# Kernel tuning notes

Hardware: AMD Instinct MI355X
Metric: run time of the kernel (lower is better)

## Reference

```python
import jax, jax.numpy as jnp
import numpy as np

B, T, D, O, E = 4, 4096, 256, 256, 16


def setup_inputs() -> dict:
    key = jax.random.key(0)
    ks = jax.random.split(key, 5)
    s_in = 1.0 / np.sqrt(D)
    x = jax.random.normal(ks[0], (B, T, D), dtype=jnp.float32)
    We = jax.random.uniform(ks[1], (E, D, O), minval=-s_in, maxval=s_in, dtype=jnp.float32)
    be = jax.random.uniform(ks[2], (E, O), minval=-s_in, maxval=s_in, dtype=jnp.float32)
    Wg = jax.random.uniform(ks[3], (D, E), minval=-s_in, maxval=s_in, dtype=jnp.float32)
    bg = jax.random.uniform(ks[4], (E,), minval=-s_in, maxval=s_in, dtype=jnp.float32)
    return {"x": x, "We": We, "be": be, "Wg": Wg, "bg": bg}


def reference(x, We, be, Wg, bg):
    # gate: softmax over experts  [B,T,E]
    gate = jax.nn.softmax(jnp.einsum("btd,de->bte", x, Wg) + bg, axis=-1)
    # all experts: batched GEMM  [B,T,E,O]
    h = jax.nn.gelu(jnp.einsum("btd,edo->bteo", x, We) + be, approximate=False)
    # softmax-weighted sum over experts  [B,T,O]
    return jnp.einsum("bteo,bte->bto", h, gate)
```

## Files before the change

### kernel.cpp

```cpp
#include <hip/hip_runtime.h>
#include <stdint.h>

#define KD 256
#define NO 256
#define NE 16
#define BM 64
#define BN 128
#define XROW 264
#define NFRAG 128

typedef short bf16x8 __attribute__((ext_vector_type(8)));
typedef float f32x4 __attribute__((ext_vector_type(4)));

__device__ __forceinline__ unsigned short f2bf(float f) {
  uint32_t u = __float_as_uint(f);
  u += 0x7fffu + ((u >> 16) & 1u);
  return (unsigned short)(u >> 16);
}
__device__ __forceinline__ float bf2f(unsigned short h) {
  return __uint_as_float(((uint32_t)h) << 16);
}
__device__ __forceinline__ float gelu_f(float h) {
  float z = h * fmaf(0.07135481627f, h * h, 1.5957691216f);
  return h * __builtin_amdgcn_rcpf(1.0f + __expf(-z));
}

__global__ void moe_prep(const float* __restrict__ We, unsigned short* __restrict__ Wf,
                         const float* __restrict__ Wg, unsigned short* __restrict__ Wgt)
{
  __shared__ float ts[256 * 17];
  const int tid = threadIdx.x;
  const int bid = blockIdx.x;
  if (bid < 256) {
    const int e = bid >> 4, ob = bid & 15;
    const float* src = We + (size_t)e * KD * NO + ob * 16;
    const int o = tid & 15, dg = tid >> 4;
#pragma unroll
    for (int p = 0; p < 16; ++p) {
      int d = p * 16 + dg;
      ts[d * 17 + o] = src[(size_t)d * NO + o];
    }
    __syncthreads();
    const int w = tid >> 6, l = tid & 63;
    const int q = l >> 4, ln = l & 15;
#pragma unroll
    for (int kk = 0; kk < 2; ++kk) {
      int kc = w + kk * 4;
      unsigned int pk[4];
#pragma unroll
      for (int h = 0; h < 4; ++h) {
        unsigned short lo = f2bf(ts[(kc * 32 + q * 8 + h * 2 + 0) * 17 + ln]);
        unsigned short hi = f2bf(ts[(kc * 32 + q * 8 + h * 2 + 1) * 17 + ln]);
        pk[h] = (unsigned int)lo | ((unsigned int)hi << 16);
      }
      uint4* dst = (uint4*)(Wf + ((((size_t)(e * 8 + kc) * 16 + ob) * 64) + l) * 8);
      *dst = make_uint4(pk[0], pk[1], pk[2], pk[3]);
    }
  } else {
    int d = tid;
    const float* wr = Wg + (size_t)d * NE;
#pragma unroll
    for (int e = 0; e < NE; ++e)
      Wgt[e * KD + d] = f2bf(wr[e]);
  }
}

__launch_bounds__(256, 2)
__global__ void moe_main(const float* __restrict__ x,
                         const uint4* __restrict__ Wf,
                         const unsigned short* __restrict__ Wgt,
                         const float* __restrict__ be,
                         const float* __restrict__ bg,
                         float* __restrict__ out)
{
  __shared__ __align__(16) unsigned short Xs[BM * XROW];
  __shared__ float gate_t[NE * 65];
  __shared__ unsigned short be_h[NE * BN];

  const int tid = threadIdx.x;
  const int bid = blockIdx.x;
  const int half = bid & 1;
  const int n0 = half * BN;
  const int m0 = (bid >> 1) * BM;
  const int w = tid >> 6, lane = tid & 63;
  const int ln = lane & 15, quad = lane >> 4;

  const int voff = (half * 8 + w * 2) * 64 + lane;

  {
    const float4* xg = (const float4*)x + (size_t)m0 * (KD / 4);
#pragma unroll
    for (int p = 0; p < 16; ++p) {
      int idx = p * 256 + tid;
      int r = idx >> 6, c = idx & 63;
      float4 v = xg[r * (KD / 4) + c];
      uint32_t lo = (uint32_t)f2bf(v.x) | ((uint32_t)f2bf(v.y) << 16);
      uint32_t hi = (uint32_t)f2bf(v.z) | ((uint32_t)f2bf(v.w) << 16);
      *(uint2*)&Xs[r * XROW + c * 4] = make_uint2(lo, hi);
    }
  }
#pragma unroll
  for (int p = 0; p < 8; ++p) {
    int idx = p * 256 + tid;
    int e = idx >> 7, c = idx & 127;
    be_h[e * BN + c] = f2bf(be[e * NO + n0 + c]);
  }
  __syncthreads();

  bf16x8 a[4][8];
#pragma unroll
  for (int i = 0; i < 4; ++i)
#pragma unroll
    for (int kc = 0; kc < 8; ++kc)
      a[i][kc] = *(const bf16x8*)&Xs[(i * 16 + ln) * XROW + kc * 32 + quad * 8];

  uint4 b[4][2];
#pragma unroll
  for (int t = 0; t < 4; ++t) {
    const uint4* p = Wf + t * 1024 + voff;
    b[t][0] = p[0]; b[t][1] = p[64];
  }

  {
    f32x4 g = {0.f, 0.f, 0.f, 0.f};
#pragma unroll
    for (int kc = 0; kc < 8; ++kc) {
      bf16x8 af = *(const bf16x8*)&Xs[(w * 16 + ln) * XROW + kc * 32 + quad * 8];
      bf16x8 wb = *(const bf16x8*)(Wgt + (size_t)ln * KD + kc * 32 + quad * 8);
      g = __builtin_amdgcn_mfma_f32_16x16x32_bf16(af, wb, g, 0, 0, 0);
    }
    float bgl = bg[ln];
#pragma unroll
    for (int r = 0; r < 4; ++r) {
      float v = g[r] + bgl;
      float mx = v;
#pragma unroll
      for (int msk = 1; msk < 16; msk <<= 1)
        mx = fmaxf(mx, __shfl_xor(mx, msk, 64));
      float ev = __expf(v - mx);
      float s = ev;
#pragma unroll
      for (int msk = 1; msk < 16; msk <<= 1)
        s += __shfl_xor(s, msk, 64);
      gate_t[ln * 65 + w * 16 + quad * 4 + r] = ev * __builtin_amdgcn_rcpf(s);
    }
  }
  __syncthreads();

  f32x4 acc[4][2], oacc[4][2];
#pragma unroll
  for (int i = 0; i < 4; ++i)
#pragma unroll
    for (int j = 0; j < 2; ++j) {
      acc[i][j] = (f32x4){0.f, 0.f, 0.f, 0.f};
      oacc[i][j] = (f32x4){0.f, 0.f, 0.f, 0.f};
    }

  const uint4* pw = Wf + 4 * 1024 + voff;

#pragma unroll 1
  for (int e = 0; e < NE; ++e) {
#pragma unroll
    for (int kc = 0; kc < 8; ++kc) {
      const int t = e * 8 + kc;
      uint4* bc = b[t & 3];
#pragma unroll
      for (int i = 0; i < 4; ++i)
#pragma unroll
        for (int j = 0; j < 2; ++j)
          acc[i][j] = __builtin_amdgcn_mfma_f32_16x16x32_bf16(
              a[i][kc], *(const bf16x8*)&bc[j], acc[i][j], 0, 0, 0);
      if (t + 4 < NFRAG) {
        bc[0] = pw[0]; bc[1] = pw[64];
        pw += 1024;
      }
    }
    {
      float gv[4][4];
#pragma unroll
      for (int i = 0; i < 4; ++i)
#pragma unroll
        for (int r = 0; r < 4; ++r)
          gv[i][r] = gate_t[e * 65 + i * 16 + quad * 4 + r];
      float bb0 = bf2f(be_h[e * BN + w * 32 + ln]);
      float bb1 = bf2f(be_h[e * BN + w * 32 + 16 + ln]);
#pragma unroll
      for (int i = 0; i < 4; ++i)
#pragma unroll
        for (int j = 0; j < 2; ++j)
#pragma unroll
          for (int r = 0; r < 4; ++r) {
            float hh = acc[i][j][r] + (j ? bb1 : bb0);
            oacc[i][j][r] = fmaf(gv[i][r], gelu_f(hh), oacc[i][j][r]);
            acc[i][j][r] = 0.f;
          }
    }
  }

#pragma unroll
  for (int i = 0; i < 4; ++i)
#pragma unroll
    for (int r = 0; r < 4; ++r) {
      int row = m0 + i * 16 + quad * 4 + r;
      float* orow = out + (size_t)row * NO + n0 + w * 32 + ln;
      orow[0]  = oacc[i][0][r];
      orow[16] = oacc[i][1][r];
    }
}

extern "C" void kernel_launch(void* const* d_in, const int* in_sizes, int n_in,
                              void* d_out, int out_size, void* d_ws, size_t ws_size,
                              hipStream_t stream) {
  const float* x  = (const float*)d_in[0];
  const float* We = (const float*)d_in[1];
  const float* be = (const float*)d_in[2];
  const float* Wg = (const float*)d_in[3];
  const float* bg = (const float*)d_in[4];
  float* out = (float*)d_out;
  unsigned short* Wf  = (unsigned short*)d_ws;
  unsigned short* Wgt = (unsigned short*)((char*)d_ws + (size_t)NE * NO * KD * 2);

  moe_prep<<<257, 256, 0, stream>>>(We, Wf, Wg, Wgt);
  moe_main<<<512, 256, 0, stream>>>(x, (const uint4*)Wf, Wgt, be, bg, out);
}
```

Measured before the change: 123.1 us.

## Prefetch a full expert of weights, rotate expert order per block, fold bias into MFMA

```diff
diff --git a/kernel.cpp b/kernel.cpp
--- a/kernel.cpp
+++ b/kernel.cpp
@@ -7,6 +7,7 @@
 #define BM 64
 #define BN 128
 #define XROW 264
+#define GROW 68
 #define NFRAG 128
 
 typedef short bf16x8 __attribute__((ext_vector_type(8)));
@@ -74,7 +75,7 @@
                          float* __restrict__ out)
 {
   __shared__ __align__(16) unsigned short Xs[BM * XROW];
-  __shared__ float gate_t[NE * 65];
+  __shared__ __align__(16) float gate_t[NE * GROW];
   __shared__ unsigned short be_h[NE * BN];
 
   const int tid = threadIdx.x;
@@ -84,6 +85,7 @@
   const int m0 = (bid >> 1) * BM;
   const int w = tid >> 6, lane = tid & 63;
   const int ln = lane & 15, quad = lane >> 4;
+  const int r0 = (bid * 5) & 15;
 
   const int voff = (half * 8 + w * 2) * 64 + lane;
 
@@ -99,6 +101,12 @@
       *(uint2*)&Xs[r * XROW + c * 4] = make_uint2(lo, hi);
     }
   }
+  uint4 b[8][2];
+#pragma unroll
+  for (int kc = 0; kc < 8; ++kc) {
+    const uint4* p = Wf + (size_t)(r0 * 8 + kc) * 1024 + voff;
+    b[kc][0] = p[0]; b[kc][1] = p[64];
+  }
 #pragma unroll
   for (int p = 0; p < 8; ++p) {
     int idx = p * 256 + tid;
@@ -114,13 +122,6 @@
     for (int kc = 0; kc < 8; ++kc)
       a[i][kc] = *(const bf16x8*)&Xs[(i * 16 + ln) * XROW + kc * 32 + quad * 8];
 
-  uint4 b[4][2];
-#pragma unroll
-  for (int t = 0; t < 4; ++t) {
-    const uint4* p = Wf + t * 1024 + voff;
-    b[t][0] = p[0]; b[t][1] = p[64];
-  }
-
   {
     f32x4 g = {0.f, 0.f, 0.f, 0.f};
 #pragma unroll
@@ -142,7 +143,7 @@
 #pragma unroll
       for (int msk = 1; msk < 16; msk <<= 1)
         s += __shfl_xor(s, msk, 64);
-      gate_t[ln * 65 + w * 16 + quad * 4 + r] = ev * __builtin_amdgcn_rcpf(s);
+      gate_t[ln * GROW + w * 16 + quad * 4 + r] = ev * __builtin_amdgcn_rcpf(s);
     }
   }
   __syncthreads();
@@ -151,49 +152,54 @@
 #pragma unroll
   for (int i = 0; i < 4; ++i)
 #pragma unroll
-    for (int j = 0; j < 2; ++j) {
-      acc[i][j] = (f32x4){0.f, 0.f, 0.f, 0.f};
+    for (int j = 0; j < 2; ++j)
       oacc[i][j] = (f32x4){0.f, 0.f, 0.f, 0.f};
-    }
-
-  const uint4* pw = Wf + 4 * 1024 + voff;
 
 #pragma unroll 1
-  for (int e = 0; e < NE; ++e) {
+  for (int ei = 0; ei < NE; ++ei) {
+    const int e = (ei + r0) & 15;
+    const int en = (ei + 1 + r0) & 15;
+    const float bb0 = bf2f(be_h[e * BN + w * 32 + ln]);
+    const float bb1 = bf2f(be_h[e * BN + w * 32 + 16 + ln]);
+    const f32x4 c0 = (f32x4){bb0, bb0, bb0, bb0};
+    const f32x4 c1 = (f32x4){bb1, bb1, bb1, bb1};
+
 #pragma unroll
     for (int kc = 0; kc < 8; ++kc) {
-      const int t = e * 8 + kc;
-      uint4* bc = b[t & 3];
+      uint4* bc = b[kc];
+      if (kc == 0) {
+#pragma unroll
+        for (int i = 0; i < 4; ++i) {
+          acc[i][0] = __builtin_amdgcn_mfma_f32_16x16x32_bf16(
+              a[i][0], *(const bf16x8*)&bc[0], c0, 0, 0, 0);
+          acc[i][1] = __builtin_amdgcn_mfma_f32_16x16x32_bf16(
+              a[i][0], *(const bf16x8*)&bc[1], c1, 0, 0, 0);
+        }
+      } else {
+#pragma unroll
+        for (int i = 0; i < 4; ++i)
+#pragma unroll
+          for (int j = 0; j < 2; ++j)
+            acc[i][j] = __builtin_amdgcn_mfma_f32_16x16x32_bf16(
+                a[i][kc], *(const bf16x8*)&bc[j], acc[i][j], 0, 0, 0);
+      }
+      if (ei < NE - 1) {
+        const uint4* p = Wf + (size_t)(en * 8 + kc) * 1024 + voff;
+        bc[0] = p[0]; bc[1] = p[64];
+      }
+    }
+    {
+      f32x4 gv[4];
 #pragma unroll
       for (int i = 0; i < 4; ++i)
+        gv[i] = *(const f32x4*)&gate_t[e * GROW + i * 16 + quad * 4];
+#pragma unroll
+      for (int i = 0; i < 4; ++i)
 #pragma unroll
         for (int j = 0; j < 2; ++j)
-          acc[i][j] = __builtin_amdgcn_mfma_f32_16x16x32_bf16(
-              a[i][kc], *(const bf16x8*)&bc[j], acc[i][j], 0, 0, 0);
-      if (t + 4 < NFRAG) {
-        bc[0] = pw[0]; bc[1] = pw[64];
-        pw += 1024;
-      }
-    }
-    {
-      float gv[4][4];
-#pragma unroll
-      for (int i = 0; i < 4; ++i)
-#pragma unroll
-        for (int r = 0; r < 4; ++r)
-          gv[i][r] = gate_t[e * 65 + i * 16 + quad * 4 + r];
-      float bb0 = bf2f(be_h[e * BN + w * 32 + ln]);
-      float bb1 = bf2f(be_h[e * BN + w * 32 + 16 + ln]);
-#pragma unroll
-      for (int i = 0; i < 4; ++i)
-#pragma unroll
-        for (int j = 0; j < 2; ++j)
-#pragma unroll
-          for (int r = 0; r < 4; ++r) {
-            float hh = acc[i][j][r] + (j ? bb1 : bb0);
-            oacc[i][j][r] = fmaf(gv[i][r], gelu_f(hh), oacc[i][j][r]);
-            acc[i][j][r] = 0.f;
-          }
+#pragma unroll
+          for (int r = 0; r < 4; ++r)
+            oacc[i][j][r] = fmaf(gv[i][r], gelu_f(acc[i][j][r]), oacc[i][j][r]);
     }
   }
 
```

New measurement: 134.2 us. 1.09x slower.

## Stagger expert order per wave, vectorize gate loads, use exp2 in GELU

Applied to the files above, without the earlier changes.

```diff
diff --git a/kernel.cpp b/kernel.cpp
--- a/kernel.cpp
+++ b/kernel.cpp
@@ -7,7 +7,7 @@
 #define BM 64
 #define BN 128
 #define XROW 264
-#define NFRAG 128
+#define GROW 68
 
 typedef short bf16x8 __attribute__((ext_vector_type(8)));
 typedef float f32x4 __attribute__((ext_vector_type(4)));
@@ -21,8 +21,13 @@
   return __uint_as_float(((uint32_t)h) << 16);
 }
 __device__ __forceinline__ float gelu_f(float h) {
+#if __has_builtin(__builtin_amdgcn_exp2f)
+  float zn = h * fmaf(-0.10294817f, h * h, -2.3022077f);
+  return h * __builtin_amdgcn_rcpf(1.0f + __builtin_amdgcn_exp2f(zn));
+#else
   float z = h * fmaf(0.07135481627f, h * h, 1.5957691216f);
   return h * __builtin_amdgcn_rcpf(1.0f + __expf(-z));
+#endif
 }
 
 __global__ void moe_prep(const float* __restrict__ We, unsigned short* __restrict__ Wf,
@@ -74,7 +79,7 @@
                          float* __restrict__ out)
 {
   __shared__ __align__(16) unsigned short Xs[BM * XROW];
-  __shared__ float gate_t[NE * 65];
+  __shared__ __align__(16) float gate_t[NE * GROW];
   __shared__ unsigned short be_h[NE * BN];
 
   const int tid = threadIdx.x;
@@ -84,6 +89,7 @@
   const int m0 = (bid >> 1) * BM;
   const int w = tid >> 6, lane = tid & 63;
   const int ln = lane & 15, quad = lane >> 4;
+  const int eoff = __builtin_amdgcn_readfirstlane(((tid >> 6) * 4 + bid) & 15);
 
   const int voff = (half * 8 + w * 2) * 64 + lane;
 
@@ -99,6 +105,12 @@
       *(uint2*)&Xs[r * XROW + c * 4] = make_uint2(lo, hi);
     }
   }
+  uint4 b[4][2];
+#pragma unroll
+  for (int kc = 0; kc < 4; ++kc) {
+    const uint4* p = Wf + ((size_t)eoff * 8 + kc) * 1024 + voff;
+    b[kc][0] = p[0]; b[kc][1] = p[64];
+  }
 #pragma unroll
   for (int p = 0; p < 8; ++p) {
     int idx = p * 256 + tid;
@@ -114,13 +126,6 @@
     for (int kc = 0; kc < 8; ++kc)
       a[i][kc] = *(const bf16x8*)&Xs[(i * 16 + ln) * XROW + kc * 32 + quad * 8];
 
-  uint4 b[4][2];
-#pragma unroll
-  for (int t = 0; t < 4; ++t) {
-    const uint4* p = Wf + t * 1024 + voff;
-    b[t][0] = p[0]; b[t][1] = p[64];
-  }
-
   {
     f32x4 g = {0.f, 0.f, 0.f, 0.f};
 #pragma unroll
@@ -142,7 +147,7 @@
 #pragma unroll
       for (int msk = 1; msk < 16; msk <<= 1)
         s += __shfl_xor(s, msk, 64);
-      gate_t[ln * 65 + w * 16 + quad * 4 + r] = ev * __builtin_amdgcn_rcpf(s);
+      gate_t[ln * GROW + w * 16 + quad * 4 + r] = ev * __builtin_amdgcn_rcpf(s);
     }
   }
   __syncthreads();
@@ -156,34 +161,37 @@
       oacc[i][j] = (f32x4){0.f, 0.f, 0.f, 0.f};
     }
 
-  const uint4* pw = Wf + 4 * 1024 + voff;
-
 #pragma unroll 1
-  for (int e = 0; e < NE; ++e) {
+  for (int ei = 0; ei < NE; ++ei) {
+    const int e  = (eoff + ei) & 15;
+    const int en = (eoff + ei + 1) & 15;
+    const uint4* bse = Wf + (size_t)e  * 8192 + voff;
+    const uint4* bsn = Wf + (size_t)en * 8192 + voff;
+
 #pragma unroll
     for (int kc = 0; kc < 8; ++kc) {
-      const int t = e * 8 + kc;
-      uint4* bc = b[t & 3];
+      uint4* bc = b[kc & 3];
 #pragma unroll
       for (int i = 0; i < 4; ++i)
 #pragma unroll
         for (int j = 0; j < 2; ++j)
           acc[i][j] = __builtin_amdgcn_mfma_f32_16x16x32_bf16(
               a[i][kc], *(const bf16x8*)&bc[j], acc[i][j], 0, 0, 0);
-      if (t + 4 < NFRAG) {
-        bc[0] = pw[0]; bc[1] = pw[64];
-        pw += 1024;
+      if (kc < 4) {
+        const uint4* p = bse + (kc + 4) * 1024;
+        bc[0] = p[0]; bc[1] = p[64];
+      } else if (ei < NE - 1) {
+        const uint4* p = bsn + (kc - 4) * 1024;
+        bc[0] = p[0]; bc[1] = p[64];
       }
     }
     {
-      float gv[4][4];
+      f32x4 gv[4];
 #pragma unroll
       for (int i = 0; i < 4; ++i)
-#pragma unroll
-        for (int r = 0; r < 4; ++r)
-          gv[i][r] = gate_t[e * 65 + i * 16 + quad * 4 + r];
-      float bb0 = bf2f(be_h[e * BN + w * 32 + ln]);
-      float bb1 = bf2f(be_h[e * BN + w * 32 + 16 + ln]);
+        gv[i] = *(const f32x4*)&gate_t[e * GROW + i * 16 + quad * 4];
+      const float bb0 = bf2f(be_h[e * BN + w * 32 + ln]);
+      const float bb1 = bf2f(be_h[e * BN + w * 32 + 16 + ln]);
 #pragma unroll
       for (int i = 0; i < 4; ++i)
 #pragma unroll
```

Result: no change. 122.0 us (-0.9%).
